# Optimization experiments

Measured on AMD Instinct MI355X. Metric: run time of the kernel, lower is better.

The kernel has to match this reference:

```python
import jax, jax.numpy as jnp
import numpy as np

NEG_INF = float(np.finfo(np.float32).min)


def setup_inputs() -> dict:
    key = jax.random.key(0)
    k1, k2, k3 = jax.random.split(key, 3)
    n_context, d_model = 4096, 2048
    x = jax.random.normal(k1, (n_context, d_model), dtype=jnp.float32)
    # nn.Linear default init scale ~ 1/sqrt(fan_in); use small weights for numeric sanity
    W_qk = jax.random.normal(k2, (d_model, d_model), dtype=jnp.float32) / np.sqrt(d_model)
    W_ov = jax.random.normal(k3, (d_model, d_model), dtype=jnp.float32) / np.sqrt(d_model)
    return {"x": x, "W_qk": W_qk, "W_ov": W_ov}


def reference(x, W_qk, W_ov):
    # Faithful to: softmax(X @ W_qk.T @ X.T + causal_mask) @ X @ W_ov.T
    # (biases of the torch Linears are never used in forward)
    n = x.shape[0]
    q = x @ W_qk.T                      # [n, d]
    scores = q @ x.T                    # [n, n]  (no 1/sqrt(d) scaling, as in source)
    causal = jnp.tril(jnp.ones((n, n), dtype=bool))
    scores = jnp.where(causal, scores, NEG_INF)  # additive -inf mask equivalent
    attn = jax.nn.softmax(scores, axis=-1)       # [n, n]
    out = (attn @ x) @ W_ov.T                    # [n, d]
    return out
```

## Files before the change

### kernel.cpp

```cpp
#include <hip/hip_runtime.h>
#include <hip/hip_bf16.h>
#include <stdint.h>
#include <stddef.h>
#include <math.h>

typedef _Float16 f16;
typedef __attribute__((ext_vector_type(8))) _Float16 f16x8;
typedef __attribute__((ext_vector_type(4))) float    f32x4;

constexpr int BM = 128, BN = 128, BK = 64;

#define GLOAD_LDS16(gp, lp)                                        \
    __builtin_amdgcn_global_load_lds(                              \
        (const __attribute__((address_space(1))) unsigned int*)(gp),\
        (__attribute__((address_space(3))) unsigned int*)(lp), 16, 0, 0)

#define MFMA_TILE(AV, BV)                                                     \
    do {                                                                      \
        __builtin_amdgcn_s_setprio(1);                                        \
        _Pragma("unroll")                                                     \
        for (int mi_ = 0; mi_ < 4; ++mi_)                                     \
            _Pragma("unroll")                                                 \
            for (int ni_ = 0; ni_ < 4; ++ni_)                                 \
                acc[mi_][ni_] = __builtin_amdgcn_mfma_f32_16x16x32_f16(       \
                    (AV)[mi_], (BV)[ni_], acc[mi_][ni_], 0, 0, 0);            \
        __builtin_amdgcn_s_setprio(0);                                        \
    } while (0)

template <int EPI>
__global__ __launch_bounds__(512, 2) void gemm8_a2(
    const f16* __restrict__ Ah, const f16* __restrict__ Al,
    const f16* __restrict__ B,
    float* __restrict__ Cf, f16* __restrict__ Co, f16* __restrict__ Clo,
    int M, int N, int K)
{
    const int bx = blockIdx.x;
    const int by = blockIdx.y;

    const int tid   = threadIdx.x;
    const int lane  = tid & 63;
    const int wave  = tid >> 6;
    const int wm    = wave >> 2;
    const int wn    = wave & 3;
    const int lrow  = lane & 15;
    const int lquad = lane >> 4;

    __shared__ f16 lds[2][32768];

    const int row0 = by * 128;
    const int col0 = bx * 256;

    const int srow = tid >> 3;
    const int scol = ((tid & 7) ^ (srow & 7)) * 8;
    const int loff = wave * 512;

    const int g0 = ((lquad)     ^ (lrow & 7)) * 8;
    const int g1 = ((4 + lquad) ^ (lrow & 7)) * 8;

    const int arow = (wm * 64 + lrow) * 64;
    const int brow = (wn * 64 + lrow) * 64 + 16384;

    const f16* gAh = Ah + (size_t)(row0 + srow) * K + scol;
    const f16* gAl = Al + (size_t)(row0 + srow) * K + scol;
    const f16* gB  = B  + (size_t)(col0 + srow) * K + scol;
    const size_t r64 = (size_t)64 * K;

    f32x4 acc[4][4];
    const f32x4 fz = {0.f, 0.f, 0.f, 0.f};
    #pragma unroll
    for (int i = 0; i < 4; ++i)
        #pragma unroll
        for (int j = 0; j < 4; ++j) acc[i][j] = fz;

    const int nt = K / 64;

    #pragma unroll
    for (int u = 0; u < 4; ++u)
        GLOAD_LDS16(gB + u * r64, &lds[0][16384 + u * 4096 + loff]);
    #pragma unroll
    for (int u = 0; u < 2; ++u)
        GLOAD_LDS16(gAh + u * r64, &lds[0][u * 4096 + loff]);
    #pragma unroll
    for (int u = 0; u < 2; ++u)
        GLOAD_LDS16(gAl + u * r64, &lds[0][8192 + u * 4096 + loff]);
    asm volatile("s_waitcnt vmcnt(2)");
    __builtin_amdgcn_s_barrier();

    auto tile_body = [&](int t, bool stage) {
        const int cur = t & 1;
        const size_t kn = (size_t)(t + 1) * 64;
        const f16* bufc = &lds[cur][0];
        f16* bufn = &lds[cur ^ 1][0];

        f16x8 av[4], bv0[4], bv1[4];

        #pragma unroll
        for (int mi = 0; mi < 4; ++mi)
            av[mi] = *(const f16x8*)&bufc[arow + mi * 1024 + g0];
        #pragma unroll
        for (int ni = 0; ni < 4; ++ni)
            bv0[ni] = *(const f16x8*)&bufc[brow + ni * 1024 + g0];
        if (stage) {
            GLOAD_LDS16(gB + kn,       &bufn[16384 + loff]);
            GLOAD_LDS16(gB + r64 + kn, &bufn[16384 + 4096 + loff]);
        }
        __builtin_amdgcn_s_barrier();
        asm volatile("s_waitcnt lgkmcnt(0)");
        MFMA_TILE(av, bv0);
        __builtin_amdgcn_s_barrier();

        #pragma unroll
        for (int mi = 0; mi < 4; ++mi)
            av[mi] = *(const f16x8*)&bufc[arow + mi * 1024 + g1];
        #pragma unroll
        for (int ni = 0; ni < 4; ++ni)
            bv1[ni] = *(const f16x8*)&bufc[brow + ni * 1024 + g1];
        if (stage) {
            GLOAD_LDS16(gB + 2 * r64 + kn, &bufn[16384 +  8192 + loff]);
            GLOAD_LDS16(gB + 3 * r64 + kn, &bufn[16384 + 12288 + loff]);
            asm volatile("s_waitcnt vmcnt(4)");
        } else {
            asm volatile("s_waitcnt vmcnt(0)");
        }
        __builtin_amdgcn_s_barrier();
        asm volatile("s_waitcnt lgkmcnt(0)");
        MFMA_TILE(av, bv1);
        __builtin_amdgcn_s_barrier();

        #pragma unroll
        for (int mi = 0; mi < 4; ++mi)
            av[mi] = *(const f16x8*)&bufc[8192 + arow + mi * 1024 + g0];
        if (stage) {
            GLOAD_LDS16(gAh + kn,       &bufn[loff]);
            GLOAD_LDS16(gAh + r64 + kn, &bufn[4096 + loff]);
        }
        __builtin_amdgcn_s_barrier();
        asm volatile("s_waitcnt lgkmcnt(0)");
        MFMA_TILE(av, bv0);
        __builtin_amdgcn_s_barrier();

        #pragma unroll
        for (int mi = 0; mi < 4; ++mi)
            av[mi] = *(const f16x8*)&bufc[8192 + arow + mi * 1024 + g1];
        if (stage) {
            GLOAD_LDS16(gAl + kn,       &bufn[ 8192 + loff]);
            GLOAD_LDS16(gAl + r64 + kn, &bufn[12288 + loff]);
        }
        asm volatile("s_waitcnt vmcnt(2)");
        __builtin_amdgcn_s_barrier();
        asm volatile("s_waitcnt lgkmcnt(0)");
        MFMA_TILE(av, bv1);
        __builtin_amdgcn_s_barrier();
    };

    for (int t = 0; t < nt - 1; ++t) tile_body(t, true);
    tile_body(nt - 1, false);

    #pragma unroll
    for (int mi = 0; mi < 4; ++mi) {
        #pragma unroll
        for (int ni = 0; ni < 4; ++ni) {
            #pragma unroll
            for (int r = 0; r < 4; ++r) {
                const int row = row0 + wm * 64 + mi * 16 + lquad * 4 + r;
                const int col = col0 + wn * 64 + ni * 16 + lrow;
                const size_t idx = (size_t)row * N + col;
                const float v = acc[mi][ni][r];
                if (EPI == 0) {
                    Cf[idx] = v;
                } else {
                    const f16 h = (f16)v;
                    Co[idx]  = h;
                    Clo[idx] = (f16)(v - (float)h);
                }
            }
        }
    }
}

__global__ __launch_bounds__(512, 2) void gemm8_s_jobs(
    const f16* __restrict__ Ah, const f16* __restrict__ Al,
    const f16* __restrict__ B,
    float* __restrict__ Cf, int N, int K)
{
    const int b = blockIdx.x;
    const int j = (b & 7) * 32 + (b >> 3);
    int r = (int)sqrtf((float)j);
    while (r * r > j) --r;
    while ((r + 1) * (r + 1) <= j) ++r;
    const int u = j - r * r;
    const int by = (u < r) ? 2 * r : 2 * r + 1;
    const int bx = (u < r) ? u : u - r;

    const int tid   = threadIdx.x;
    const int lane  = tid & 63;
    const int wave  = tid >> 6;
    const int wm    = wave >> 2;
    const int wn    = wave & 3;
    const int lrow  = lane & 15;
    const int lquad = lane >> 4;

    __shared__ f16 lds[2][32768];

    const int row0 = by * 128;
    const int col0 = bx * 256;

    const int srow = tid >> 3;
    const int scol = ((tid & 7) ^ (srow & 7)) * 8;
    const int loff = wave * 512;

    const int g0 = ((lquad)     ^ (lrow & 7)) * 8;
    const int g1 = ((4 + lquad) ^ (lrow & 7)) * 8;

    const int arow = (wm * 64 + lrow) * 64;
    const int brow = (wn * 64 + lrow) * 64 + 16384;

    const f16* gAh = Ah + (size_t)(row0 + srow) * K + scol;
    const f16* gAl = Al + (size_t)(row0 + srow) * K + scol;
    const f16* gB  = B  + (size_t)(col0 + srow) * K + scol;
    const size_t r64 = (size_t)64 * K;

    f32x4 acc[4][4];
    const f32x4 fz = {0.f, 0.f, 0.f, 0.f};
    #pragma unroll
    for (int i = 0; i < 4; ++i)
        #pragma unroll
        for (int jj = 0; jj < 4; ++jj) acc[i][jj] = fz;

    const int nt = K / 64;

    #pragma unroll
    for (int u2 = 0; u2 < 4; ++u2)
        GLOAD_LDS16(gB + u2 * r64, &lds[0][16384 + u2 * 4096 + loff]);
    #pragma unroll
    for (int u2 = 0; u2 < 2; ++u2)
        GLOAD_LDS16(gAh + u2 * r64, &lds[0][u2 * 4096 + loff]);
    #pragma unroll
    for (int u2 = 0; u2 < 2; ++u2)
        GLOAD_LDS16(gAl + u2 * r64, &lds[0][8192 + u2 * 4096 + loff]);
    asm volatile("s_waitcnt vmcnt(2)");
    __builtin_amdgcn_s_barrier();

    auto tile_body = [&](int t, bool stage) {
        const int cur = t & 1;
        const size_t kn = (size_t)(t + 1) * 64;
        const f16* bufc = &lds[cur][0];
        f16* bufn = &lds[cur ^ 1][0];

        f16x8 av[4], bv0[4], bv1[4];

        #pragma unroll
        for (int mi = 0; mi < 4; ++mi)
            av[mi] = *(const f16x8*)&bufc[arow + mi * 1024 + g0];
        #pragma unroll
        for (int ni = 0; ni < 4; ++ni)
            bv0[ni] = *(const f16x8*)&bufc[brow + ni * 1024 + g0];
        if (stage) {
            GLOAD_LDS16(gB + kn,       &bufn[16384 + loff]);
            GLOAD_LDS16(gB + r64 + kn, &bufn[16384 + 4096 + loff]);
        }
        __builtin_amdgcn_s_barrier();
        asm volatile("s_waitcnt lgkmcnt(0)");
        MFMA_TILE(av, bv0);
        __builtin_amdgcn_s_barrier();

        #pragma unroll
        for (int mi = 0; mi < 4; ++mi)
            av[mi] = *(const f16x8*)&bufc[arow + mi * 1024 + g1];
        #pragma unroll
        for (int ni = 0; ni < 4; ++ni)
            bv1[ni] = *(const f16x8*)&bufc[brow + ni * 1024 + g1];
        if (stage) {
            GLOAD_LDS16(gB + 2 * r64 + kn, &bufn[16384 +  8192 + loff]);
            GLOAD_LDS16(gB + 3 * r64 + kn, &bufn[16384 + 12288 + loff]);
            asm volatile("s_waitcnt vmcnt(4)");
        } else {
            asm volatile("s_waitcnt vmcnt(0)");
        }
        __builtin_amdgcn_s_barrier();
        asm volatile("s_waitcnt lgkmcnt(0)");
        MFMA_TILE(av, bv1);
        __builtin_amdgcn_s_barrier();

        #pragma unroll
        for (int mi = 0; mi < 4; ++mi)
            av[mi] = *(const f16x8*)&bufc[8192 + arow + mi * 1024 + g0];
        if (stage) {
            GLOAD_LDS16(gAh + kn,       &bufn[loff]);
            GLOAD_LDS16(gAh + r64 + kn, &bufn[4096 + loff]);
        }
        __builtin_amdgcn_s_barrier();
        asm volatile("s_waitcnt lgkmcnt(0)");
        MFMA_TILE(av, bv0);
        __builtin_amdgcn_s_barrier();

        #pragma unroll
        for (int mi = 0; mi < 4; ++mi)
            av[mi] = *(const f16x8*)&bufc[8192 + arow + mi * 1024 + g1];
        if (stage) {
            GLOAD_LDS16(gAl + kn,       &bufn[ 8192 + loff]);
            GLOAD_LDS16(gAl + r64 + kn, &bufn[12288 + loff]);
        }
        asm volatile("s_waitcnt vmcnt(2)");
        __builtin_amdgcn_s_barrier();
        asm volatile("s_waitcnt lgkmcnt(0)");
        MFMA_TILE(av, bv1);
        __builtin_amdgcn_s_barrier();
    };

    for (int t = 0; t < nt - 1; ++t) tile_body(t, true);
    tile_body(nt - 1, false);

    #pragma unroll
    for (int mi = 0; mi < 4; ++mi) {
        #pragma unroll
        for (int ni = 0; ni < 4; ++ni) {
            #pragma unroll
            for (int rr = 0; rr < 4; ++rr) {
                const int row = row0 + wm * 64 + mi * 16 + lquad * 4 + rr;
                const int col = col0 + wn * 64 + ni * 16 + lrow;
                Cf[(size_t)row * N + col] = acc[mi][ni][rr];
            }
        }
    }
}

__global__ __launch_bounds__(256) void gemm_half_splitk(
    const f16* __restrict__ Ah, const f16* __restrict__ Al,
    const f16* __restrict__ B, float* __restrict__ Spart, int Kg)
{
    const int kc = blockIdx.x;
    const int h  = blockIdx.y;
    const int row0 = h * 256;
    const int kbeg = kc * 256;

    const int tid   = threadIdx.x;
    const int lane  = tid & 63;
    const int wave  = tid >> 6;
    const int wm    = wave >> 1;
    const int wn    = wave & 1;
    const int lrow  = lane & 15;
    const int lquad = lane >> 4;

    __shared__ f16 sAh[BM * BK];
    __shared__ f16 sAl[BM * BK];
    __shared__ f16 sB [BM * BK];

    const int srow = tid >> 3;
    const int scol = (((tid & 7) ^ ((tid >> 3) & 7))) * 8;
    const int lbase = wave * 512;

    f32x4 acc[4][4];
    const f32x4 fz = {0.f, 0.f, 0.f, 0.f};
    #pragma unroll
    for (int i = 0; i < 4; ++i)
        #pragma unroll
        for (int jj = 0; jj < 4; ++jj) acc[i][jj] = fz;

    for (int k0 = kbeg; k0 < kbeg + 256; k0 += BK) {
        __syncthreads();
        #pragma unroll
        for (int r = 0; r < 4; ++r) {
            const int trow = srow + 32 * r;
            const size_t ga = (size_t)(row0 + trow) * Kg + k0 + scol;
            const int ldst = lbase + r * 2048;
            GLOAD_LDS16(&Ah[ga], &sAh[ldst]);
            GLOAD_LDS16(&Al[ga], &sAl[ldst]);
            GLOAD_LDS16(&B [ga], &sB [ldst]);
        }
        __syncthreads();

        #pragma unroll
        for (int kk = 0; kk < 2; ++kk) {
            const int grpA = ((kk * 4 + lquad) ^ (lrow & 7)) * 8;
            f16x8 ah[4], al[4], bv[4];
            #pragma unroll
            for (int mi = 0; mi < 4; ++mi) {
                const int off = (wm * 64 + mi * 16 + lrow) * BK + grpA;
                ah[mi] = *reinterpret_cast<const f16x8*>(&sAh[off]);
                al[mi] = *reinterpret_cast<const f16x8*>(&sAl[off]);
            }
            #pragma unroll
            for (int ni = 0; ni < 4; ++ni)
                bv[ni] = *reinterpret_cast<const f16x8*>(
                    &sB[(wn * 64 + ni * 16 + lrow) * BK + grpA]);

            #pragma unroll
            for (int mi = 0; mi < 4; ++mi)
                #pragma unroll
                for (int ni = 0; ni < 4; ++ni) {
                    acc[mi][ni] = __builtin_amdgcn_mfma_f32_16x16x32_f16(
                        ah[mi], bv[ni], acc[mi][ni], 0, 0, 0);
                    acc[mi][ni] = __builtin_amdgcn_mfma_f32_16x16x32_f16(
                        al[mi], bv[ni], acc[mi][ni], 0, 0, 0);
                }
        }
    }

    float* out = Spart + ((size_t)(kc * 16 + h)) * (128 * 128);
    #pragma unroll
    for (int mi = 0; mi < 4; ++mi) {
        #pragma unroll
        for (int ni = 0; ni < 4; ++ni) {
            #pragma unroll
            for (int r = 0; r < 4; ++r) {
                const int row = wm * 64 + mi * 16 + lquad * 4 + r;
                const int col = wn * 64 + ni * 16 + lrow;
                out[row * 128 + col] = acc[mi][ni][r];
            }
        }
    }
}

__global__ __launch_bounds__(256) void combine_halves(
    const float* __restrict__ Spart, float* __restrict__ S, int n)
{
    const int h = blockIdx.y;
    const int e = (blockIdx.x * 256 + threadIdx.x) * 4;
    float4 a = *reinterpret_cast<const float4*>(
        &Spart[(size_t)h * (128 * 128) + e]);
    #pragma unroll
    for (int kc = 1; kc < 8; ++kc) {
        const float4 b = *reinterpret_cast<const float4*>(
            &Spart[(size_t)(kc * 16 + h) * (128 * 128) + e]);
        a.x += b.x; a.y += b.y; a.z += b.z; a.w += b.w;
    }
    const int i = e >> 7, jj = e & 127;
    *reinterpret_cast<float4*>(&S[(size_t)(h * 256 + i) * n + h * 256 + jj]) = a;
}

template <int EPI>
__global__ __launch_bounds__(512, 2) void gemm8_1t(
    const f16* __restrict__ A, const f16* __restrict__ B,
    float* __restrict__ Cf, f16* __restrict__ Co,
    int M, int N, int K)
{
    const int bx = blockIdx.x;
    const int by = blockIdx.y;

    const int tid   = threadIdx.x;
    const int lane  = tid & 63;
    const int wave  = tid >> 6;
    const int wm    = wave >> 2;
    const int wn    = wave & 3;
    const int lrow  = lane & 15;
    const int lquad = lane >> 4;

    __shared__ f16 lds[3][24576];

    const int row0 = by * 128;
    const int col0 = bx * 256;

    const int srow = tid >> 3;
    const int scol = ((tid & 7) ^ (srow & 7)) * 8;
    const int loff = wave * 512;
    const int g0 = ((lquad)     ^ (lrow & 7)) * 8;
    const int g1 = ((4 + lquad) ^ (lrow & 7)) * 8;
    const int arow = (wm * 64 + lrow) * 64;
    const int brow = (wn * 64 + lrow) * 64 + 8192;

    const f16* gA = A + (size_t)(row0 + srow) * K + scol;
    const f16* gB = B + (size_t)(col0 + srow) * K + scol;
    const size_t r64 = (size_t)64 * K;

    f32x4 acc[4][4];
    const f32x4 fz = {0.f, 0.f, 0.f, 0.f};
    #pragma unroll
    for (int i = 0; i < 4; ++i)
        #pragma unroll
        for (int j = 0; j < 4; ++j) acc[i][j] = fz;

    const int nt = K / 64;

    #pragma unroll
    for (int tt = 0; tt < 2; ++tt) {
        const size_t kk = (size_t)tt * 64;
        #pragma unroll
        for (int u = 0; u < 4; ++u)
            GLOAD_LDS16(gB + u * r64 + kk, &lds[tt][8192 + u * 4096 + loff]);
        #pragma unroll
        for (int u = 0; u < 2; ++u)
            GLOAD_LDS16(gA + u * r64 + kk, &lds[tt][u * 4096 + loff]);
    }
    asm volatile("s_waitcnt vmcnt(6)");
    __builtin_amdgcn_s_barrier();

    int cur = 0;
    for (int t = 0; t < nt; ++t) {
        const int nb = (cur >= 1) ? (cur - 1) : (cur + 2);
        const bool stage2 = (t + 2 < nt);
        const size_t kn = (size_t)(t + 2) * 64;
        const f16* bufc = &lds[cur][0];
        f16* bufn = &lds[nb][0];

        f16x8 av[4], bv[4];

        #pragma unroll
        for (int mi = 0; mi < 4; ++mi)
            av[mi] = *(const f16x8*)&bufc[arow + mi * 1024 + g0];
        #pragma unroll
        for (int ni = 0; ni < 4; ++ni)
            bv[ni] = *(const f16x8*)&bufc[brow + ni * 1024 + g0];
        if (stage2) {
            GLOAD_LDS16(gB + kn,           &bufn[8192 + loff]);
            GLOAD_LDS16(gB + r64 + kn,     &bufn[8192 + 4096 + loff]);
            GLOAD_LDS16(gB + 2 * r64 + kn, &bufn[8192 + 8192 + loff]);
        }
        __builtin_amdgcn_s_barrier();
        asm volatile("s_waitcnt lgkmcnt(0)");
        MFMA_TILE(av, bv);
        __builtin_amdgcn_s_barrier();

        #pragma unroll
        for (int mi = 0; mi < 4; ++mi)
            av[mi] = *(const f16x8*)&bufc[arow + mi * 1024 + g1];
        #pragma unroll
        for (int ni = 0; ni < 4; ++ni)
            bv[ni] = *(const f16x8*)&bufc[brow + ni * 1024 + g1];
        if (stage2) {
            GLOAD_LDS16(gB + 3 * r64 + kn, &bufn[8192 + 12288 + loff]);
            GLOAD_LDS16(gA + kn,           &bufn[loff]);
            GLOAD_LDS16(gA + r64 + kn,     &bufn[4096 + loff]);
            asm volatile("s_waitcnt vmcnt(6)");
        } else {
            asm volatile("s_waitcnt vmcnt(0)");
        }
        __builtin_amdgcn_s_barrier();
        asm volatile("s_waitcnt lgkmcnt(0)");
        MFMA_TILE(av, bv);
        __builtin_amdgcn_s_barrier();

        cur = (cur == 2) ? 0 : cur + 1;
    }

    #pragma unroll
    for (int mi = 0; mi < 4; ++mi) {
        #pragma unroll
        for (int ni = 0; ni < 4; ++ni) {
            #pragma unroll
            for (int r = 0; r < 4; ++r) {
                const int row = row0 + wm * 64 + mi * 16 + lquad * 4 + r;
                const int col = col0 + wn * 64 + ni * 16 + lrow;
                const size_t idx = (size_t)row * N + col;
                const float v = acc[mi][ni][r];
                if (EPI == 0) Cf[idx] = v;
                else          Co[idx] = (f16)v;
            }
        }
    }
}

template <int EPI, bool KCAUSAL>
__global__ __launch_bounds__(256) void gemm_plain(
    const f16* __restrict__ A, const f16* __restrict__ B,
    float* __restrict__ Cf, f16* __restrict__ Co,
    int M, int N, int K)
{
    const int bx = blockIdx.x;
    const int by = KCAUSAL ? (gridDim.y - 1 - blockIdx.y) : blockIdx.y;

    const int tid   = threadIdx.x;
    const int lane  = tid & 63;
    const int wave  = tid >> 6;
    const int wm    = wave >> 1;
    const int wn    = wave & 1;
    const int lrow  = lane & 15;
    const int lquad = lane >> 4;

    __shared__ f16 sA[BM * BK];
    __shared__ f16 sB[BN * BK];

    const int row0 = by * BM;
    const int col0 = bx * BN;

    const int srow = tid >> 3;
    const int scol = (((tid & 7) ^ ((tid >> 3) & 7))) * 8;
    const int lbase = wave * 512;

    f32x4 acc[4][4];
    const f32x4 fzero = {0.f, 0.f, 0.f, 0.f};
    #pragma unroll
    for (int i = 0; i < 4; ++i)
        #pragma unroll
        for (int j = 0; j < 4; ++j) acc[i][j] = fzero;

    const int Keff = KCAUSAL ? (by + 1) * BM : K;

    for (int k0 = 0; k0 < Keff; k0 += BK) {
        __syncthreads();
        #pragma unroll
        for (int r = 0; r < 4; ++r) {
            const int trow = srow + 32 * r;
            GLOAD_LDS16(&A[(size_t)(row0 + trow) * K + k0 + scol], &sA[lbase + r * 2048]);
            GLOAD_LDS16(&B[(size_t)(col0 + trow) * K + k0 + scol], &sB[lbase + r * 2048]);
        }
        __syncthreads();

        #pragma unroll
        for (int kk = 0; kk < 2; ++kk) {
            const int grpA = ((kk * 4 + lquad) ^ (lrow & 7)) * 8;
            f16x8 av[4], bv[4];
            #pragma unroll
            for (int mi = 0; mi < 4; ++mi)
                av[mi] = *reinterpret_cast<const f16x8*>(
                    &sA[(wm * 64 + mi * 16 + lrow) * BK + grpA]);
            #pragma unroll
            for (int ni = 0; ni < 4; ++ni)
                bv[ni] = *reinterpret_cast<const f16x8*>(
                    &sB[(wn * 64 + ni * 16 + lrow) * BK + grpA]);

            #pragma unroll
            for (int mi = 0; mi < 4; ++mi)
                #pragma unroll
                for (int ni = 0; ni < 4; ++ni)
                    acc[mi][ni] = __builtin_amdgcn_mfma_f32_16x16x32_f16(
                        av[mi], bv[ni], acc[mi][ni], 0, 0, 0);
        }
    }

    #pragma unroll
    for (int mi = 0; mi < 4; ++mi) {
        #pragma unroll
        for (int ni = 0; ni < 4; ++ni) {
            #pragma unroll
            for (int r = 0; r < 4; ++r) {
                const int row = row0 + wm * 64 + mi * 16 + lquad * 4 + r;
                const int col = col0 + wn * 64 + ni * 16 + lrow;
                const size_t idx = (size_t)row * N + col;
                const float v = acc[mi][ni][r];
                if (EPI == 0) Cf[idx] = v;
                else          Co[idx] = (f16)v;
            }
        }
    }
}

__global__ __launch_bounds__(256) void split_f32_f16(
    const float* __restrict__ in, f16* __restrict__ hi, f16* __restrict__ lo,
    size_t nelem)
{
    const size_t i = ((size_t)blockIdx.x * 256 + threadIdx.x) * 4;
    if (i >= nelem) return;
    const float4 v = *reinterpret_cast<const float4*>(in + i);
    union { f16 h[4]; ushort4 u; } H, L;
    H.h[0] = (f16)v.x; H.h[1] = (f16)v.y; H.h[2] = (f16)v.z; H.h[3] = (f16)v.w;
    *reinterpret_cast<ushort4*>(hi + i) = H.u;
    if (lo) {
        L.h[0] = (f16)(v.x - (float)H.h[0]);
        L.h[1] = (f16)(v.y - (float)H.h[1]);
        L.h[2] = (f16)(v.z - (float)H.h[2]);
        L.h[3] = (f16)(v.w - (float)H.h[3]);
        *reinterpret_cast<ushort4*>(lo + i) = L.u;
    }
}

__global__ __launch_bounds__(256) void softmax_rows(
    const float* __restrict__ S, f16* __restrict__ P, int n)
{
    const int row = blockIdx.x;
    const int len = row + 1;
    const int padlen = ((row >> 7) + 1) << 7;
    const float* srow = S + (size_t)row * n;
    f16* prow = P + (size_t)row * n;
    const int tid = threadIdx.x;
    const int lane = tid & 63, wave = tid >> 6;
    __shared__ float rowbuf[4096];
    __shared__ float redm[4], reds[4];

    float m = -3.0e38f, s = 0.f;
    for (int j = tid; j < len; j += 256) {
        const float v = srow[j];
        rowbuf[j] = v;
        const float mn = fmaxf(m, v);
        s = s * __expf(m - mn) + __expf(v - mn);
        m = mn;
    }
    #pragma unroll
    for (int off = 32; off; off >>= 1) {
        const float mo = __shfl_xor(m, off, 64);
        const float so = __shfl_xor(s, off, 64);
        const float mn = fmaxf(m, mo);
        s = s * __expf(m - mn) + so * __expf(mo - mn);
        m = mn;
    }
    if (lane == 0) { redm[wave] = m; reds[wave] = s; }
    __syncthreads();
    float M = redm[0], Sm = reds[0];
    #pragma unroll
    for (int w = 1; w < 4; ++w) {
        const float mn = fmaxf(M, redm[w]);
        Sm = Sm * __expf(M - mn) + reds[w] * __expf(redm[w] - mn);
        M = mn;
    }
    const float inv = 1.0f / Sm;

    const f16 z = (f16)0.0f;
    for (int j = tid; j < padlen; j += 256)
        prow[j] = (j < len) ? (f16)(__expf(rowbuf[j] - M) * inv) : z;
}

__global__ __launch_bounds__(256) void transpose_f32_f16(
    const float* __restrict__ in, f16* __restrict__ out, int rows, int cols)
{
    __shared__ float tile[32][33];
    const int bx = blockIdx.x;
    const int by = blockIdx.y;
    const int tx = threadIdx.x & 31;
    const int ty = threadIdx.x >> 5;
    #pragma unroll
    for (int r = 0; r < 4; ++r)
        tile[ty + 8 * r][tx] = in[(size_t)(by * 32 + ty + 8 * r) * cols + bx * 32 + tx];
    __syncthreads();
    #pragma unroll
    for (int r = 0; r < 4; ++r)
        out[(size_t)(bx * 32 + ty + 8 * r) * rows + by * 32 + tx] =
            (f16)tile[tx][ty + 8 * r];
}

extern "C" void kernel_launch(void* const* d_in, const int* in_sizes, int n_in,
                              void* d_out, int out_size, void* d_ws, size_t ws_size,
                              hipStream_t stream)
{
    const int n = 4096, d = 2048;
    const float* x   = (const float*)d_in[0];
    const float* Wqk = (const float*)d_in[1];
    const float* Wov = (const float*)d_in[2];
    float* out = (float*)d_out;

    char* ws = (char*)d_ws;
    const size_t MB = 1 << 20;
    f16*   xh   = (f16*)  (ws);
    f16*   xl   = (f16*)  (ws + 16 * MB);
    f16*   Wh   = (f16*)  (ws + 32 * MB);
    f16*   Wovh = (f16*)  (ws + 40 * MB);
    f16*   xTh  = (f16*)  (ws + 48 * MB);
    f16*   qh   = (f16*)  (ws + 64 * MB);
    f16*   ql   = (f16*)  (ws + 80 * MB);
    float* S    = (float*)(ws + 96 * MB);
    float* Sp   = (float*)(ws + 16 * MB);
    f16*   P    = (f16*)  (ws);
    f16*   o    = (f16*)  (ws + 64 * MB);

    const dim3 blk(256);
    const dim3 blk8(512);

    split_f32_f16<<<dim3((n * d) / (256 * 4)), blk, 0, stream>>>(x,   xh, xl, (size_t)n * d);
    split_f32_f16<<<dim3((d * d) / (256 * 4)), blk, 0, stream>>>(Wqk, Wh, nullptr, (size_t)d * d);
    split_f32_f16<<<dim3((d * d) / (256 * 4)), blk, 0, stream>>>(Wov, Wovh, nullptr, (size_t)d * d);
    transpose_f32_f16<<<dim3(d / 32, n / 32), blk, 0, stream>>>(x, xTh, n, d);

    gemm8_a2<1><<<dim3(d / 256, n / 128), blk8, 0, stream>>>(
        xh, xl, Wh, nullptr, qh, ql, n, d, d);

    gemm8_s_jobs<<<dim3(256), blk8, 0, stream>>>(qh, ql, xh, S, n, d);
    gemm_half_splitk<<<dim3(8, 16), blk, 0, stream>>>(qh, ql, xh, Sp, d);
    combine_halves<<<dim3(16, 16), blk, 0, stream>>>(Sp, S, n);

    softmax_rows<<<dim3(n), blk, 0, stream>>>(S, P, n);

    gemm_plain<2, true><<<dim3(d / BN, n / BM), blk, 0, stream>>>(
        P, xTh, nullptr, o, n, d, n);

    gemm8_1t<0><<<dim3(d / 256, n / 128), blk8, 0, stream>>>(
        o, Wovh, out, nullptr, n, d, d);
}
```

Before: 399.5 us.

## Use pipelined 8-wave GEMM for causal P@X and fuse x prep kernels

The causal P@X product moves from the simple single-buffered 256-thread GEMM to the triple-buffered 512-thread 128x256 tile GEMM. A KCAUSAL template parameter limits the K range per row block and launches the heaviest blocks first. The x hi/lo split and the x transpose are merged into one prep kernel, so x is read once instead of twice. Risks: larger tiles give fewer blocks and more imbalance across the causal triangle, and the prep kernel's hi/lo writes are less coalesced than the vectorised split.

Measured after the change: 380.4 us. -4.8%, faster.

```diff
diff --git a/kernel.cpp b/kernel.cpp
--- a/kernel.cpp
+++ b/kernel.cpp
@@ -397,7 +397,7 @@
         }
     }
 
-    float* out = Spart + ((size_t)(kc * 16 + h)) * (128 * 128);
+    float* outp = Spart + ((size_t)(kc * 16 + h)) * (128 * 128);
     #pragma unroll
     for (int mi = 0; mi < 4; ++mi) {
         #pragma unroll
@@ -406,7 +406,7 @@
             for (int r = 0; r < 4; ++r) {
                 const int row = wm * 64 + mi * 16 + lquad * 4 + r;
                 const int col = wn * 64 + ni * 16 + lrow;
-                out[row * 128 + col] = acc[mi][ni][r];
+                outp[row * 128 + col] = acc[mi][ni][r];
             }
         }
     }
@@ -429,14 +429,14 @@
     *reinterpret_cast<float4*>(&S[(size_t)(h * 256 + i) * n + h * 256 + jj]) = a;
 }
 
-template <int EPI>
+template <int EPI, bool KCAUSAL>
 __global__ __launch_bounds__(512, 2) void gemm8_1t(
     const f16* __restrict__ A, const f16* __restrict__ B,
     float* __restrict__ Cf, f16* __restrict__ Co,
     int M, int N, int K)
 {
     const int bx = blockIdx.x;
-    const int by = blockIdx.y;
+    const int by = KCAUSAL ? ((int)gridDim.y - 1 - (int)blockIdx.y) : blockIdx.y;
 
     const int tid   = threadIdx.x;
     const int lane  = tid & 63;
@@ -470,7 +470,8 @@
         #pragma unroll
         for (int j = 0; j < 4; ++j) acc[i][j] = fz;
 
-    const int nt = K / 64;
+    const int Keff = KCAUSAL ? (by + 1) * 128 : K;
+    const int nt = Keff / 64;
 
     #pragma unroll
     for (int tt = 0; tt < 2; ++tt) {
@@ -531,91 +532,6 @@
         __builtin_amdgcn_s_barrier();
 
         cur = (cur == 2) ? 0 : cur + 1;
-    }
-
-    #pragma unroll
-    for (int mi = 0; mi < 4; ++mi) {
-        #pragma unroll
-        for (int ni = 0; ni < 4; ++ni) {
-            #pragma unroll
-            for (int r = 0; r < 4; ++r) {
-                const int row = row0 + wm * 64 + mi * 16 + lquad * 4 + r;
-                const int col = col0 + wn * 64 + ni * 16 + lrow;
-                const size_t idx = (size_t)row * N + col;
-                const float v = acc[mi][ni][r];
-                if (EPI == 0) Cf[idx] = v;
-                else          Co[idx] = (f16)v;
-            }
-        }
-    }
-}
-
-template <int EPI, bool KCAUSAL>
-__global__ __launch_bounds__(256) void gemm_plain(
-    const f16* __restrict__ A, const f16* __restrict__ B,
-    float* __restrict__ Cf, f16* __restrict__ Co,
-    int M, int N, int K)
-{
-    const int bx = blockIdx.x;
-    const int by = KCAUSAL ? (gridDim.y - 1 - blockIdx.y) : blockIdx.y;
-
-    const int tid   = threadIdx.x;
-    const int lane  = tid & 63;
-    const int wave  = tid >> 6;
-    const int wm    = wave >> 1;
-    const int wn    = wave & 1;
-    const int lrow  = lane & 15;
-    const int lquad = lane >> 4;
-
-    __shared__ f16 sA[BM * BK];
-    __shared__ f16 sB[BN * BK];
-
-    const int row0 = by * BM;
-    const int col0 = bx * BN;
-
-    const int srow = tid >> 3;
-    const int scol = (((tid & 7) ^ ((tid >> 3) & 7))) * 8;
-    const int lbase = wave * 512;
-
-    f32x4 acc[4][4];
-    const f32x4 fzero = {0.f, 0.f, 0.f, 0.f};
-    #pragma unroll
-    for (int i = 0; i < 4; ++i)
-        #pragma unroll
-        for (int j = 0; j < 4; ++j) acc[i][j] = fzero;
-
-    const int Keff = KCAUSAL ? (by + 1) * BM : K;
-
-    for (int k0 = 0; k0 < Keff; k0 += BK) {
-        __syncthreads();
-        #pragma unroll
-        for (int r = 0; r < 4; ++r) {
-            const int trow = srow + 32 * r;
-            GLOAD_LDS16(&A[(size_t)(row0 + trow) * K + k0 + scol], &sA[lbase + r * 2048]);
-            GLOAD_LDS16(&B[(size_t)(col0 + trow) * K + k0 + scol], &sB[lbase + r * 2048]);
-        }
-        __syncthreads();
-
-        #pragma unroll
-        for (int kk = 0; kk < 2; ++kk) {
-            const int grpA = ((kk * 4 + lquad) ^ (lrow & 7)) * 8;
-            f16x8 av[4], bv[4];
-            #pragma unroll
-            for (int mi = 0; mi < 4; ++mi)
-                av[mi] = *reinterpret_cast<const f16x8*>(
-                    &sA[(wm * 64 + mi * 16 + lrow) * BK + grpA]);
-            #pragma unroll
-            for (int ni = 0; ni < 4; ++ni)
-                bv[ni] = *reinterpret_cast<const f16x8*>(
-                    &sB[(wn * 64 + ni * 16 + lrow) * BK + grpA]);
-
-            #pragma unroll
-            for (int mi = 0; mi < 4; ++mi)
-                #pragma unroll
-                for (int ni = 0; ni < 4; ++ni)
-                    acc[mi][ni] = __builtin_amdgcn_mfma_f32_16x16x32_f16(
-                        av[mi], bv[ni], acc[mi][ni], 0, 0, 0);
-        }
     }
 
     #pragma unroll
@@ -654,6 +570,32 @@
     }
 }
 
+__global__ __launch_bounds__(256) void prep_x(
+    const float* __restrict__ in, f16* __restrict__ hi, f16* __restrict__ lo,
+    f16* __restrict__ tr, int rows, int cols)
+{
+    __shared__ float tile[32][33];
+    const int bx = blockIdx.x;
+    const int by = blockIdx.y;
+    const int tx = threadIdx.x & 31;
+    const int ty = threadIdx.x >> 5;
+    #pragma unroll
+    for (int r = 0; r < 4; ++r) {
+        const int row = by * 32 + ty + 8 * r;
+        const int col = bx * 32 + tx;
+        const float v = in[(size_t)row * cols + col];
+        tile[ty + 8 * r][tx] = v;
+        const f16 h = (f16)v;
+        hi[(size_t)row * cols + col] = h;
+        lo[(size_t)row * cols + col] = (f16)(v - (float)h);
+    }
+    __syncthreads();
+    #pragma unroll
+    for (int r = 0; r < 4; ++r)
+        tr[(size_t)(bx * 32 + ty + 8 * r) * rows + by * 32 + tx] =
+            (f16)tile[tx][ty + 8 * r];
+}
+
 __global__ __launch_bounds__(256) void softmax_rows(
     const float* __restrict__ S, f16* __restrict__ P, int n)
 {
@@ -697,24 +639,6 @@
     const f16 z = (f16)0.0f;
     for (int j = tid; j < padlen; j += 256)
         prow[j] = (j < len) ? (f16)(__expf(rowbuf[j] - M) * inv) : z;
-}
-
-__global__ __launch_bounds__(256) void transpose_f32_f16(
-    const float* __restrict__ in, f16* __restrict__ out, int rows, int cols)
-{
-    __shared__ float tile[32][33];
-    const int bx = blockIdx.x;
-    const int by = blockIdx.y;
-    const int tx = threadIdx.x & 31;
-    const int ty = threadIdx.x >> 5;
-    #pragma unroll
-    for (int r = 0; r < 4; ++r)
-        tile[ty + 8 * r][tx] = in[(size_t)(by * 32 + ty + 8 * r) * cols + bx * 32 + tx];
-    __syncthreads();
-    #pragma unroll
-    for (int r = 0; r < 4; ++r)
-        out[(size_t)(bx * 32 + ty + 8 * r) * rows + by * 32 + tx] =
-            (f16)tile[tx][ty + 8 * r];
 }
 
 extern "C" void kernel_launch(void* const* d_in, const int* in_sizes, int n_in,
@@ -744,10 +668,9 @@
     const dim3 blk(256);
     const dim3 blk8(512);
 
-    split_f32_f16<<<dim3((n * d) / (256 * 4)), blk, 0, stream>>>(x,   xh, xl, (size_t)n * d);
     split_f32_f16<<<dim3((d * d) / (256 * 4)), blk, 0, stream>>>(Wqk, Wh, nullptr, (size_t)d * d);
     split_f32_f16<<<dim3((d * d) / (256 * 4)), blk, 0, stream>>>(Wov, Wovh, nullptr, (size_t)d * d);
-    transpose_f32_f16<<<dim3(d / 32, n / 32), blk, 0, stream>>>(x, xTh, n, d);
+    prep_x<<<dim3(d / 32, n / 32), blk, 0, stream>>>(x, xh, xl, xTh, n, d);
 
     gemm8_a2<1><<<dim3(d / 256, n / 128), blk8, 0, stream>>>(
         xh, xl, Wh, nullptr, qh, ql, n, d, d);
@@ -758,9 +681,9 @@
 
     softmax_rows<<<dim3(n), blk, 0, stream>>>(S, P, n);
 
-    gemm_plain<2, true><<<dim3(d / BN, n / BM), blk, 0, stream>>>(
+    gemm8_1t<2, true><<<dim3(d / 256, n / 128), blk8, 0, stream>>>(
         P, xTh, nullptr, o, n, d, n);
 
-    gemm8_1t<0><<<dim3(d / 256, n / 128), blk8, 0, stream>>>(
+    gemm8_1t<0, false><<<dim3(d / 256, n / 128), blk8, 0, stream>>>(
         o, Wovh, out, nullptr, n, d, d);
 }
```
